# Performance work log

Hardware: AMD Instinct MI355X
Metric: run time of the kernel (lower is better)

## Reference

```python
import jax, jax.numpy as jnp
import numpy as np

THETA = 0.5
ALPHA = 2.1
OMEGA = 14.0
EPS = 1.0


def setup_inputs() -> dict:
    key = jax.random.key(0)
    k1, k2 = jax.random.split(key)
    shape = (8, 1, 128, 256, 256)  # (B, C, D, H, W) 3D heatmap volumes
    inp = jax.random.uniform(k1, shape, dtype=jnp.float32)
    target = jax.random.uniform(k2, shape, dtype=jnp.float32)
    return {"input": inp, "target": target}


def reference(input, target):
    # Adaptive Wing loss (Wang et al., ICCV 2019), faithful to the torch module.
    # NOTE: the scipy binary_opening mask in the original is identically 1 for all
    # inputs (bool-array assignment `img_dilate[img_dilate < 51] = 1` sets everything
    # to True), so the mask multiply is a no-op and is omitted here.
    p = ALPHA - target                      # exponent, in (1.1, 2.1]
    ratio = THETA / EPS
    t = jnp.power(ratio, p)                 # (theta/eps)^(alpha - target)
    A = OMEGA * (1.0 / (1.0 + t)) * p * jnp.power(ratio, p - 1.0) * (1.0 / EPS)
    C = THETA * A - OMEGA * jnp.log1p(t)
    diff = jnp.abs(target - input)
    linear = A * diff - C
    nonlinear = OMEGA * jnp.log1p(jnp.power(diff / EPS, p))
    loss = jnp.where(diff < THETA, nonlinear, linear)
    return jnp.sum(loss)  # reduction='sum'
```

## Files before the change

kernel.cpp:

```cpp
#include <hip/hip_runtime.h>


#define LN2_X14 9.704060527839234f

__device__ __forceinline__ float awl_elem(float x, float tg) {
    float p = 2.1f - tg;
    float t = __builtin_amdgcn_exp2f(-p);
    float A = 28.0f * p * t * __builtin_amdgcn_rcpf(1.0f + t);
    float diff = fabsf(tg - x);
    float q = __builtin_amdgcn_exp2f(p * __builtin_amdgcn_logf(diff));
    bool lt = diff < 0.5f;
    float z = lt ? q : t;
    float extra = lt ? 0.0f : A * (diff - 0.5f);
    return fmaf(LN2_X14, __builtin_amdgcn_logf(1.0f + z), extra);
}

__device__ __forceinline__ float awl_quad(float4 a, float4 b) {
    return (awl_elem(a.x, b.x) + awl_elem(a.y, b.y))
         + (awl_elem(a.z, b.z) + awl_elem(a.w, b.w));
}

__global__ __launch_bounds__(256) void awl_partial(
    const float4* __restrict__ x, const float4* __restrict__ tg,
    float* __restrict__ part, int n4)
{
    int tid = blockIdx.x * blockDim.x + threadIdx.x;
    int stride = gridDim.x * blockDim.x;
    int lane = threadIdx.x & 63;
    int wave_base = ((tid >> 6) << 7) + lane;
    float acc = 0.0f;

    int s = 0;
    for (; s + 2 * stride <= n4; s += 2 * stride) {
        int i0 = s + wave_base;
        int i1 = i0 + 64;
        float4 a0 = x[i0];
        float4 a1 = x[i1];
        float4 b0 = tg[i0];
        float4 b1 = tg[i1];
        acc += awl_quad(a0, b0);
        acc += awl_quad(a1, b1);
    }
    for (int i = s + tid; i < n4; i += stride)
        acc += awl_quad(x[i], tg[i]);

    #pragma unroll
    for (int off = 32; off > 0; off >>= 1)
        acc += __shfl_down(acc, off, 64);
    __shared__ float ws[4];
    int wid = threadIdx.x >> 6;
    if (lane == 0) ws[wid] = acc;
    __syncthreads();
    if (threadIdx.x == 0)
        part[blockIdx.x] = (ws[0] + ws[1]) + (ws[2] + ws[3]);
}

__global__ __launch_bounds__(256) void awl_final(
    const float* __restrict__ part, int n, float* __restrict__ out)
{
    float acc = 0.0f;
    for (int i = threadIdx.x; i < n; i += 256) acc += part[i];
    #pragma unroll
    for (int off = 32; off > 0; off >>= 1)
        acc += __shfl_down(acc, off, 64);
    __shared__ float ws[4];
    int lane = threadIdx.x & 63;
    int wid  = threadIdx.x >> 6;
    if (lane == 0) ws[wid] = acc;
    __syncthreads();
    if (threadIdx.x == 0)
        out[0] = (ws[0] + ws[1]) + (ws[2] + ws[3]);
}

extern "C" void kernel_launch(void* const* d_in, const int* in_sizes, int n_in,
                              void* d_out, int out_size, void* d_ws, size_t ws_size,
                              hipStream_t stream) {
    const float* x  = (const float*)d_in[0];
    const float* tg = (const float*)d_in[1];
    float* out  = (float*)d_out;
    float* part = (float*)d_ws;

    long long n = (long long)in_sizes[0];
    int n4 = (int)(n / 4);

    int nblk = 2048;
    int cap = (int)(ws_size / sizeof(float));
    if (cap > 0 && nblk > cap) nblk = cap;
    if (nblk < 1) nblk = 1;

    awl_partial<<<nblk, 256, 0, stream>>>((const float4*)x, (const float4*)tg, part, n4);
    awl_final<<<1, 256, 0, stream>>>(part, nblk, out);
}
```

Baseline: 98.01 us.

## Replace linear-branch transcendentals with polynomials, unroll loads 4x, atomic final reduction

Replaces the exp2/rcp/log work for the linear branch with quartic polynomial fits in the target value for A and the constant term, leaving one log/exp2/log chain for the nonlinear branch. It widens the main loop to four float4 loads per input per iteration for more memory-level parallelism. It also drops the second reduction kernel in favour of a memset plus a per-block atomicAdd. The polynomial fits are approximations of the exact formulas over the target range [0,1], and the atomic sum makes the result order nondeterministic.

```diff
diff --git a/kernel.cpp b/kernel.cpp
--- a/kernel.cpp
+++ b/kernel.cpp
@@ -4,15 +4,16 @@
 #define LN2_X14 9.704060527839234f
 
 __device__ __forceinline__ float awl_elem(float x, float tg) {
+    float diff = fabsf(tg - x);
     float p = 2.1f - tg;
-    float t = __builtin_amdgcn_exp2f(-p);
-    float A = 28.0f * p * t * __builtin_amdgcn_rcpf(1.0f + t);
-    float diff = fabsf(tg - x);
-    float q = __builtin_amdgcn_exp2f(p * __builtin_amdgcn_logf(diff));
-    bool lt = diff < 0.5f;
-    float z = lt ? q : t;
-    float extra = lt ? 0.0f : A * (diff - 0.5f);
-    return fmaf(LN2_X14, __builtin_amdgcn_logf(1.0f + z), extra);
+    float q  = __builtin_amdgcn_exp2f(p * __builtin_amdgcn_logf(diff));
+    float nl = LN2_X14 * __builtin_amdgcn_logf(1.0f + q);
+    float A = fmaf(fmaf(fmaf(fmaf(-0.0054016f, tg, -0.6702400f), tg,
+                             -1.5973632f), tg, 0.9491764f), tg, 11.1215496f);
+    float L = fmaf(fmaf(fmaf(fmaf(-0.0032405f, tg, 0.0785600f), tg,
+                             0.5144176f), tg, 1.8354348f), tg, 2.9352736f);
+    float lin = fmaf(A, diff - 0.5f, L);
+    return diff < 0.5f ? nl : lin;
 }
 
 __device__ __forceinline__ float awl_quad(float4 a, float4 b) {
@@ -20,26 +21,32 @@
          + (awl_elem(a.z, b.z) + awl_elem(a.w, b.w));
 }
 
-__global__ __launch_bounds__(256) void awl_partial(
+__global__ __launch_bounds__(256) void awl_sum(
     const float4* __restrict__ x, const float4* __restrict__ tg,
-    float* __restrict__ part, int n4)
+    float* __restrict__ out, int n4)
 {
-    int tid = blockIdx.x * blockDim.x + threadIdx.x;
+    int tid    = blockIdx.x * blockDim.x + threadIdx.x;
     int stride = gridDim.x * blockDim.x;
-    int lane = threadIdx.x & 63;
-    int wave_base = ((tid >> 6) << 7) + lane;
+    int lane   = threadIdx.x & 63;
+    int wbase  = ((tid >> 6) << 8) + lane;
+    int step   = stride << 2;
     float acc = 0.0f;
 
     int s = 0;
-    for (; s + 2 * stride <= n4; s += 2 * stride) {
-        int i0 = s + wave_base;
-        int i1 = i0 + 64;
+    for (; s + step <= n4; s += step) {
+        int i0 = s + wbase;
         float4 a0 = x[i0];
-        float4 a1 = x[i1];
+        float4 a1 = x[i0 + 64];
+        float4 a2 = x[i0 + 128];
+        float4 a3 = x[i0 + 192];
         float4 b0 = tg[i0];
-        float4 b1 = tg[i1];
+        float4 b1 = tg[i0 + 64];
+        float4 b2 = tg[i0 + 128];
+        float4 b3 = tg[i0 + 192];
         acc += awl_quad(a0, b0);
         acc += awl_quad(a1, b1);
+        acc += awl_quad(a2, b2);
+        acc += awl_quad(a3, b3);
     }
     for (int i = s + tid; i < n4; i += stride)
         acc += awl_quad(x[i], tg[i]);
@@ -52,24 +59,7 @@
     if (lane == 0) ws[wid] = acc;
     __syncthreads();
     if (threadIdx.x == 0)
-        part[blockIdx.x] = (ws[0] + ws[1]) + (ws[2] + ws[3]);
-}
-
-__global__ __launch_bounds__(256) void awl_final(
-    const float* __restrict__ part, int n, float* __restrict__ out)
-{
-    float acc = 0.0f;
-    for (int i = threadIdx.x; i < n; i += 256) acc += part[i];
-    #pragma unroll
-    for (int off = 32; off > 0; off >>= 1)
-        acc += __shfl_down(acc, off, 64);
-    __shared__ float ws[4];
-    int lane = threadIdx.x & 63;
-    int wid  = threadIdx.x >> 6;
-    if (lane == 0) ws[wid] = acc;
-    __syncthreads();
-    if (threadIdx.x == 0)
-        out[0] = (ws[0] + ws[1]) + (ws[2] + ws[3]);
+        atomicAdd(out, (ws[0] + ws[1]) + (ws[2] + ws[3]));
 }
 
 extern "C" void kernel_launch(void* const* d_in, const int* in_sizes, int n_in,
@@ -77,17 +67,13 @@
                               hipStream_t stream) {
     const float* x  = (const float*)d_in[0];
     const float* tg = (const float*)d_in[1];
-    float* out  = (float*)d_out;
-    float* part = (float*)d_ws;
+    float* out = (float*)d_out;
 
     long long n = (long long)in_sizes[0];
     int n4 = (int)(n / 4);
 
     int nblk = 2048;
-    int cap = (int)(ws_size / sizeof(float));
-    if (cap > 0 && nblk > cap) nblk = cap;
-    if (nblk < 1) nblk = 1;
 
-    awl_partial<<<nblk, 256, 0, stream>>>((const float4*)x, (const float4*)tg, part, n4);
-    awl_final<<<1, 256, 0, stream>>>(part, nblk, out);
+    hipMemsetAsync(out, 0, sizeof(float) * (out_size > 0 ? out_size : 1), stream);
+    awl_sum<<<nblk, 256, 0, stream>>>((const float4*)x, (const float4*)tg, out, n4);
 }
```

New measurement: 112.0 us. 1.14x slower.
